# Optimization experiments

Measured on AMD Instinct MI355X. Metric: run time of the kernel, lower is better.

## Reference

```python
import jax, jax.numpy as jnp
import numpy as np

HIDDEN = 512
HEAD = 64
SEQ = 2048
CHUNK = 256
GAMMA = 0.96875
SCALE_BASE = 512.0


def _xpos(x, downscale):
    # x: [B, L, hd]; XPOS with offset=0 (scale rows == length, no trimming needed)
    B, L, hd = x.shape
    half = hd // 2
    scale_vec = (jnp.arange(0, hd, 2, dtype=jnp.float32) + 0.4 * hd) / (1.4 * hd)  # [half]
    power = jnp.arange(L, dtype=jnp.float32) / SCALE_BASE                          # [L]
    scale = scale_vec[None, :] ** power[:, None]                                   # [L, half]
    inv_freq = 1.0 / (10000.0 ** (jnp.arange(half, dtype=jnp.float32) / half))
    sinusoid = jnp.arange(L, dtype=jnp.float32)[:, None] * inv_freq[None, :]       # [L, half]
    sin, cos = jnp.sin(sinusoid), jnp.cos(sinusoid)
    if downscale:
        scale = 1.0 / scale
    # duplicate_interleave: repeat each column twice -> [L, hd]
    sin_f = jnp.repeat(sin * scale, 2, axis=-1)
    cos_f = jnp.repeat(cos * scale, 2, axis=-1)
    x1 = x[:, :, 0::2]
    x2 = x[:, :, 1::2]
    rot = jnp.stack((-x2, x1), axis=-1).reshape(B, L, hd)  # rotate_every_two
    return x * cos_f + rot * sin_f


def _D_parallel():
    # D[i, j] = gamma^|i-j| if j < (i//chunk + 1)*chunk else 0 (block-causal with in-chunk lookahead)
    i = jnp.arange(SEQ)[:, None]
    j = jnp.arange(SEQ)[None, :]
    j_max = (i // CHUNK + 1) * CHUNK
    decay = GAMMA ** jnp.abs(i - j).astype(jnp.float32)
    return jnp.where(j < j_max, decay, 0.0)  # gamma>0 so no NaNs to scrub


def setup_inputs() -> dict:
    key = jax.random.key(0)
    k1, k2, k3, k4 = jax.random.split(key, 4)
    X = jax.random.normal(k1, (8, SEQ, HIDDEN), dtype=jnp.float32)
    W_Q = jax.random.normal(k2, (HIDDEN, HEAD), dtype=jnp.float32) / HIDDEN
    W_K = jax.random.normal(k3, (HIDDEN, HEAD), dtype=jnp.float32) / HIDDEN
    W_V = jax.random.normal(k4, (HIDDEN, HEAD), dtype=jnp.float32) / HIDDEN
    return {"X": X, "W_Q": W_Q, "W_K": W_K, "W_V": W_V}


def reference(X, W_Q, W_K, W_V):
    Q = _xpos(X @ W_Q, downscale=False)   # [B, S, H]
    K = _xpos(X @ W_K, downscale=True)    # [B, S, H]
    V = X @ W_V                           # [B, S, V]
    D = _D_parallel()                     # [S, S]
    scores = jnp.einsum('bqh,bkh->bqk', Q, K) * D[None]
    return jnp.einsum('bqk,bkv->bqv', scores, V)
```

## Files before the change

kernel.cpp:

```cpp
#include <hip/hip_runtime.h>
#include <hip/hip_bf16.h>


typedef __attribute__((ext_vector_type(8))) short short8;
typedef __attribute__((ext_vector_type(4))) float floatx4;

#define LOG2GAMMA (-0.04580350f)

static __device__ __forceinline__ unsigned short f2bf(float f) {
    __hip_bfloat16 h = __float2bfloat16(f);
    return *reinterpret_cast<unsigned short*>(&h);
}


__global__ __launch_bounds__(256) void prep_kernel(
    const float* __restrict__ Wq, const float* __restrict__ Wk,
    const float* __restrict__ Wv,
    __hip_bfloat16* __restrict__ Wfrag, float* __restrict__ tabs)
{
    int idx = blockIdx.x * 256 + threadIdx.x;
    const int WF_N = 192 * 512;
    if (idx < WF_N) {
        int j    = idx & 7;
        int n15  = (idx >> 3) & 15;
        int quad = (idx >> 7) & 3;
        int kkg  = (idx >> 9) & 15;
        int tile = idx >> 13;
        int n = tile * 16 + n15;
        int k = kkg * 32 + quad * 8 + j;
        int m = n >> 6, c = n & 63;
        const float* W = (m == 0) ? Wq : ((m == 1) ? Wk : Wv);
        Wfrag[idx] = __float2bfloat16(W[k * 64 + c]);
    } else {
        int t2 = idx - WF_N;
        if (t2 < 4 * 2048 * 32) {
            int tab = t2 >> 16;
            int rem = t2 & 65535;
            int pos = rem >> 5;
            int t   = rem & 31;
            float inv_freq = powf(10000.0f, -(float)t / 32.0f);
            float sinus = (float)pos * inv_freq;
            float s = sinf(sinus), c = cosf(sinus);
            float sv = (2.0f * (float)t + 0.4f * 64.0f) / (1.4f * 64.0f);
            float power = (float)pos / 512.0f;
            float scl = powf(sv, (tab >= 2) ? -power : power);
            tabs[t2] = ((tab & 1) == 0) ? c * scl : s * scl;
        }
    }
}

__global__ __launch_bounds__(256, 4) void proj_kernel(
    const float* __restrict__ X, const __hip_bfloat16* __restrict__ Wfrag,
    const float* __restrict__ tabs,
    __hip_bfloat16* __restrict__ Qfrag, __hip_bfloat16* __restrict__ Kfrag,
    __hip_bfloat16* __restrict__ Vfrag)
{
    __shared__ __hip_bfloat16 smem[32 * 520];

    int tid = threadIdx.x;
    int r0 = blockIdx.x * 32;
    int w = tid >> 6, lane = tid & 63, quad = lane >> 4, l15 = lane & 15;
    int rh = w & 1, nh = w >> 1;

#pragma unroll
    for (int u = 0; u < 16; u++) {
        int f = u * 256 + tid;
        int row = f >> 7, c = f & 127;
        float4 v = *(const float4*)(X + (r0 + row) * 512 + c * 4);
        ushort4 pk;
        pk.x = f2bf(v.x); pk.y = f2bf(v.y); pk.z = f2bf(v.z); pk.w = f2bf(v.w);
        *(ushort4*)&smem[row * 520 + c * 4] = pk;
    }
    __syncthreads();

    floatx4 acc[6];
#pragma unroll
    for (int t = 0; t < 6; t++) acc[t] = (floatx4){0.f, 0.f, 0.f, 0.f};

#pragma unroll
    for (int ks = 0; ks < 16; ks++) {
        short8 a = *(const short8*)&smem[(rh * 16 + l15) * 520 + ks * 32 + quad * 8];
#pragma unroll
        for (int t = 0; t < 6; t++) {
            int tile = nh * 6 + t;
            short8 bfr = *(const short8*)(Wfrag + ((tile * 16 + ks) * 64 + lane) * 8);
            acc[t] = __builtin_amdgcn_mfma_f32_16x16x32_bf16(a, bfr, acc[t], 0, 0, 0);
        }
    }
    __syncthreads();

    __hip_bfloat16* bufQ = smem;
    __hip_bfloat16* bufK = smem + 2304;
    __hip_bfloat16* bufV = smem + 4608;
    int b = r0 >> 11, n0 = r0 & 2047;
    int rrow = rh * 16 + quad * 4;

#pragma unroll
    for (int tl = 0; tl < 6; tl++) {
        int t = nh * 6 + tl;
#pragma unroll
        for (int rg = 0; rg < 4; rg++) {
            int row = rrow + rg;
            int n = n0 + row;
            float val = acc[tl][rg];
            float prt = __shfl_xor(val, 1, 64);
            if (t < 4) {
                int ch = t * 16 + l15, tt = ch >> 1;
                float co = tabs[n * 32 + tt];
                float si = tabs[65536 + n * 32 + tt];
                float o = (l15 & 1) ? (val * co + prt * si) : (val * co - prt * si);
                bufQ[row * 72 + ch] = __float2bfloat16(o);
            } else if (t < 8) {
                int ch = (t - 4) * 16 + l15, tt = ch >> 1;
                float co = tabs[131072 + n * 32 + tt];
                float si = tabs[196608 + n * 32 + tt];
                float o = (l15 & 1) ? (val * co + prt * si) : (val * co - prt * si);
                bufK[row * 72 + ch] = __float2bfloat16(o);
            } else {
                int ch = (t - 8) * 16 + l15;
                bufV[ch * 40 + row] = __float2bfloat16(val);
            }
        }
    }
    __syncthreads();

    {
        int tile2 = tid >> 7, kk = (tid >> 6) & 1, ln = tid & 63;
        int q2 = ln >> 4, m15 = ln & 15;
        size_t qkbase = ((((size_t)b * 128 + (n0 >> 4) + tile2) * 2 + kk) * 64 + ln) * 8;
        uint4 vq = *(const uint4*)&bufQ[(tile2 * 16 + m15) * 72 + kk * 32 + q2 * 8];
        *(uint4*)(Qfrag + qkbase) = vq;
        uint4 vk = *(const uint4*)&bufK[(tile2 * 16 + m15) * 72 + kk * 32 + q2 * 8];
        *(uint4*)(Kfrag + qkbase) = vk;
        int t2 = tid >> 6;
        uint4 vv = *(const uint4*)&bufV[(t2 * 16 + m15) * 40 + q2 * 8];
        *(uint4*)(Vfrag + ((((size_t)b * 64 + (n0 >> 5)) * 4 + t2) * 64 + ln) * 8) = vv;
    }
}

__global__ __launch_bounds__(256, 3) void attn_kernel(
    const __hip_bfloat16* __restrict__ Qfrag, const __hip_bfloat16* __restrict__ Kfrag,
    const __hip_bfloat16* __restrict__ Vfrag, float* __restrict__ out)
{
    __shared__ __hip_bfloat16 lp[4][16 * 264];

    int tid = threadIdx.x;
    int b = blockIdx.x >> 6, qt = blockIdx.x & 63;
    int q0 = qt * 32, qc = q0 >> 8;
    int w = tid >> 6, lane = tid & 63, quad = lane >> 4, l15 = lane & 15;
    int qh = w >> 1, h = w & 1;
    int qt16 = (q0 >> 4) + qh;

    short8 qf[2];
#pragma unroll
    for (int kk = 0; kk < 2; kk++)
        qf[kk] = *(const short8*)(Qfrag + ((((size_t)b * 128 + qt16) * 2 + kk) * 64 + lane) * 8);

    __hip_bfloat16* P = &lp[w][0];

    floatx4 o[4];
#pragma unroll
    for (int t = 0; t < 4; t++) o[t] = (floatx4){0.f, 0.f, 0.f, 0.f};

    int kc0 = (qc >= 3) ? (qc - 3) : 0;
    for (int kc = kc0 + h; kc <= qc; kc += 2) {
        floatx4 s[16];
#pragma unroll
        for (int t = 0; t < 16; t++) s[t] = (floatx4){0.f, 0.f, 0.f, 0.f};
#pragma unroll
        for (int t = 0; t < 16; t++) {
#pragma unroll
            for (int kk = 0; kk < 2; kk++) {
                short8 bfr = *(const short8*)(Kfrag +
                    ((((size_t)b * 128 + kc * 16 + t) * 2 + kk) * 64 + lane) * 8);
                s[t] = __builtin_amdgcn_mfma_f32_16x16x32_bf16(qf[kk], bfr, s[t], 0, 0, 0);
            }
        }

        int i0 = q0 + qh * 16 + quad * 4;
        int kbase = kc * 256;
#pragma unroll
        for (int t = 0; t < 16; t++) {
            int j = kbase + t * 16 + l15;
#pragma unroll
            for (int rg = 0; rg < 4; rg++) {
                int d = i0 + rg - j; d = (d < 0) ? -d : d;
                float p = s[t][rg] * exp2f(LOG2GAMMA * (float)d);
                P[(quad * 4 + rg) * 264 + t * 16 + l15] = __float2bfloat16(p);
            }
        }

#pragma unroll
        for (int ks = 0; ks < 8; ks++) {
            short8 a = *(const short8*)&P[l15 * 264 + ks * 32 + quad * 8];
#pragma unroll
            for (int t2 = 0; t2 < 4; t2++) {
                short8 bfr = *(const short8*)(Vfrag +
                    ((((size_t)b * 64 + kc * 8 + ks) * 4 + t2) * 64 + lane) * 8);
                o[t2] = __builtin_amdgcn_mfma_f32_16x16x32_bf16(a, bfr, o[t2], 0, 0, 0);
            }
        }
    }

    float* mine = (float*)&lp[w][0];
    float* part = (float*)&lp[w ^ 1][0];
    if (h == 1) {
#pragma unroll
        for (int t2 = 0; t2 < 4; t2++)
#pragma unroll
            for (int rg = 0; rg < 4; rg++)
                mine[(quad * 4 + rg) * 64 + t2 * 16 + l15] = o[t2][rg];
    }
    __syncthreads();
    if (h == 0) {
        int rbase = b * 2048 + q0 + qh * 16 + quad * 4;
#pragma unroll
        for (int t2 = 0; t2 < 4; t2++)
#pragma unroll
            for (int rg = 0; rg < 4; rg++)
                out[(size_t)(rbase + rg) * 64 + t2 * 16 + l15] =
                    o[t2][rg] + part[(quad * 4 + rg) * 64 + t2 * 16 + l15];
    }
}

extern "C" void kernel_launch(void* const* d_in, const int* in_sizes, int n_in,
                              void* d_out, int out_size, void* d_ws, size_t ws_size,
                              hipStream_t stream) {
    const float* X  = (const float*)d_in[0];
    const float* Wq = (const float*)d_in[1];
    const float* Wk = (const float*)d_in[2];
    const float* Wv = (const float*)d_in[3];
    float* out = (float*)d_out;

    char* ws = (char*)d_ws;
    __hip_bfloat16* Wfrag = (__hip_bfloat16*)(ws);
    float*          tabs  = (float*)(ws + 196608);
    __hip_bfloat16* Qfrag = (__hip_bfloat16*)(ws + 1245184);
    __hip_bfloat16* Kfrag = (__hip_bfloat16*)(ws + 3342336);
    __hip_bfloat16* Vfrag = (__hip_bfloat16*)(ws + 5439488);

    prep_kernel<<<1408, 256, 0, stream>>>(Wq, Wk, Wv, Wfrag, tabs);
    proj_kernel<<<512, 256, 0, stream>>>(X, Wfrag, tabs, Qfrag, Kfrag, Vfrag);
    attn_kernel<<<512, 256, 0, stream>>>(Qfrag, Kfrag, Vfrag, out);
}
```

Baseline: 128.2 us.

## Replace off-diagonal chunk attention with chunkwise recurrent KV state

Attention is reformulated in the retention style. Each chunk's decayed K^T V state is precomputed by a new zk kernel. The attention kernel then handles only the diagonal chunk explicitly and adds contributions from up to three previous chunks through a decay-scaled Q times a combined state, summed with gamma^256 weights. This removes most of the off-diagonal QK and PV MFMA work, at the cost of an extra launch, extra workspace, and bf16 rounding of the decayed K and the combined state, which adds precision risk.

New measurement: 111.8 us. -12.8%, faster.

```diff
diff --git a/kernel.cpp b/kernel.cpp
--- a/kernel.cpp
+++ b/kernel.cpp
@@ -6,6 +6,7 @@
 typedef __attribute__((ext_vector_type(4))) float floatx4;
 
 #define LOG2GAMMA (-0.04580350f)
+#define GINV      (1.0f / 0.96875f)
 
 static __device__ __forceinline__ unsigned short f2bf(float f) {
     __hip_bfloat16 h = __float2bfloat16(f);
@@ -53,7 +54,8 @@
     const float* __restrict__ X, const __hip_bfloat16* __restrict__ Wfrag,
     const float* __restrict__ tabs,
     __hip_bfloat16* __restrict__ Qfrag, __hip_bfloat16* __restrict__ Kfrag,
-    __hip_bfloat16* __restrict__ Vfrag)
+    __hip_bfloat16* __restrict__ Vfrag, __hip_bfloat16* __restrict__ Qsfrag,
+    __hip_bfloat16* __restrict__ Ktfrag)
 {
     __shared__ __hip_bfloat16 smem[32 * 520];
 
@@ -89,9 +91,10 @@
     }
     __syncthreads();
 
-    __hip_bfloat16* bufQ = smem;
-    __hip_bfloat16* bufK = smem + 2304;
-    __hip_bfloat16* bufV = smem + 4608;
+    __hip_bfloat16* bufQ  = smem;
+    __hip_bfloat16* bufK  = smem + 2304;
+    __hip_bfloat16* bufV  = smem + 4608;
+    __hip_bfloat16* bufQs = smem + 7168;
     int b = r0 >> 11, n0 = r0 & 2047;
     int rrow = rh * 16 + quad * 4;
 
@@ -110,6 +113,8 @@
                 float si = tabs[65536 + n * 32 + tt];
                 float o = (l15 & 1) ? (val * co + prt * si) : (val * co - prt * si);
                 bufQ[row * 72 + ch] = __float2bfloat16(o);
+                float qs = exp2f(LOG2GAMMA * (float)((n & 255) + 1));
+                bufQs[row * 72 + ch] = __float2bfloat16(o * qs);
             } else if (t < 8) {
                 int ch = (t - 4) * 16 + l15, tt = ch >> 1;
                 float co = tabs[131072 + n * 32 + tt];
@@ -130,96 +135,186 @@
         size_t qkbase = ((((size_t)b * 128 + (n0 >> 4) + tile2) * 2 + kk) * 64 + ln) * 8;
         uint4 vq = *(const uint4*)&bufQ[(tile2 * 16 + m15) * 72 + kk * 32 + q2 * 8];
         *(uint4*)(Qfrag + qkbase) = vq;
+        uint4 vqs = *(const uint4*)&bufQs[(tile2 * 16 + m15) * 72 + kk * 32 + q2 * 8];
+        *(uint4*)(Qsfrag + qkbase) = vqs;
         uint4 vk = *(const uint4*)&bufK[(tile2 * 16 + m15) * 72 + kk * 32 + q2 * 8];
         *(uint4*)(Kfrag + qkbase) = vk;
         int t2 = tid >> 6;
         uint4 vv = *(const uint4*)&bufV[(t2 * 16 + m15) * 40 + q2 * 8];
         *(uint4*)(Vfrag + ((((size_t)b * 64 + (n0 >> 5)) * 4 + t2) * 64 + ln) * 8) = vv;
     }
-}
-
-__global__ __launch_bounds__(256, 3) void attn_kernel(
+    {
+        int wdt = tid >> 6, ln2 = tid & 63;
+        int q2 = ln2 >> 4, m15 = ln2 & 15;
+        int jb0 = (n0 & 255) + q2 * 8;
+        float sc = exp2f(LOG2GAMMA * (float)(255 - jb0));
+        short8 pk;
+#pragma unroll
+        for (int jj = 0; jj < 8; jj++) {
+            float v = __bfloat162float(bufK[(q2 * 8 + jj) * 72 + wdt * 16 + m15]) * sc;
+            pk[jj] = (short)f2bf(v);
+            sc *= GINV;
+        }
+        int c = n0 >> 8, ksg = (n0 >> 5) & 7;
+        *(short8*)(Ktfrag + ((((size_t)(b * 8 + c) * 4 + wdt) * 8 + ksg) * 64 + ln2) * 8) = pk;
+    }
+}
+
+__global__ __launch_bounds__(256, 2) void zk_kernel(
+    const __hip_bfloat16* __restrict__ Ktfrag,
+    const __hip_bfloat16* __restrict__ Vfrag, float* __restrict__ Zf)
+{
+    __shared__ float zz[64 * 68];
+
+    int tid = threadIdx.x;
+    int b = blockIdx.x >> 3, c = blockIdx.x & 7;
+    int w = tid >> 6, lane = tid & 63, quad = lane >> 4, l15 = lane & 15;
+
+    floatx4 acc[4];
+#pragma unroll
+    for (int t = 0; t < 4; t++) acc[t] = (floatx4){0.f, 0.f, 0.f, 0.f};
+
+#pragma unroll
+    for (int ks = 0; ks < 8; ks++) {
+        short8 a = *(const short8*)(Ktfrag +
+            ((((size_t)(b * 8 + c) * 4 + w) * 8 + ks) * 64 + lane) * 8);
+#pragma unroll
+        for (int vt = 0; vt < 4; vt++) {
+            short8 bfr = *(const short8*)(Vfrag +
+                ((((size_t)b * 64 + c * 8 + ks) * 4 + vt) * 64 + lane) * 8);
+            acc[vt] = __builtin_amdgcn_mfma_f32_16x16x32_bf16(a, bfr, acc[vt], 0, 0, 0);
+        }
+    }
+#pragma unroll
+    for (int vt = 0; vt < 4; vt++)
+#pragma unroll
+        for (int rg = 0; rg < 4; rg++)
+            zz[(w * 16 + quad * 4 + rg) * 68 + vt * 16 + l15] = acc[vt][rg];
+    __syncthreads();
+
+    {
+        int vt = tid >> 6;
+#pragma unroll
+        for (int kk = 0; kk < 2; kk++) {
+            float v[8];
+#pragma unroll
+            for (int jd = 0; jd < 8; jd++)
+                v[jd] = zz[(kk * 32 + quad * 8 + jd) * 68 + vt * 16 + l15];
+            float* zp = Zf + (((((size_t)(b * 8 + c) * 4 + vt) * 2 + kk) * 64 + lane) * 8);
+            *(float4*)zp       = (float4){v[0], v[1], v[2], v[3]};
+            *(float4*)(zp + 4) = (float4){v[4], v[5], v[6], v[7]};
+        }
+    }
+}
+
+__global__ __launch_bounds__(128, 4) void attn_kernel(
     const __hip_bfloat16* __restrict__ Qfrag, const __hip_bfloat16* __restrict__ Kfrag,
-    const __hip_bfloat16* __restrict__ Vfrag, float* __restrict__ out)
+    const __hip_bfloat16* __restrict__ Vfrag, const __hip_bfloat16* __restrict__ Qsfrag,
+    const float* __restrict__ Zf, float* __restrict__ out)
 {
-    __shared__ __hip_bfloat16 lp[4][16 * 264];
+    __shared__ __hip_bfloat16 P[2 * 16 * 132];
+    __shared__ float obuf[16 * 68];
 
     int tid = threadIdx.x;
-    int b = blockIdx.x >> 6, qt = blockIdx.x & 63;
-    int q0 = qt * 32, qc = q0 >> 8;
-    int w = tid >> 6, lane = tid & 63, quad = lane >> 4, l15 = lane & 15;
-    int qh = w >> 1, h = w & 1;
-    int qt16 = (q0 >> 4) + qh;
+    int b = blockIdx.x >> 7, qt = blockIdx.x & 127;
+    int qc = qt >> 4;
+    int h = tid >> 6, lane = tid & 63, quad = lane >> 4, l15 = lane & 15;
+    __hip_bfloat16* Pw = P + h * 2112;
 
     short8 qf[2];
 #pragma unroll
     for (int kk = 0; kk < 2; kk++)
-        qf[kk] = *(const short8*)(Qfrag + ((((size_t)b * 128 + qt16) * 2 + kk) * 64 + lane) * 8);
-
-    __hip_bfloat16* P = &lp[w][0];
+        qf[kk] = *(const short8*)(Qfrag + (((size_t)(b * 128 + qt) * 2 + kk) * 64 + lane) * 8);
 
     floatx4 o[4];
 #pragma unroll
     for (int t = 0; t < 4; t++) o[t] = (floatx4){0.f, 0.f, 0.f, 0.f};
 
-    int kc0 = (qc >= 3) ? (qc - 3) : 0;
-    for (int kc = kc0 + h; kc <= qc; kc += 2) {
-        floatx4 s[16];
-#pragma unroll
-        for (int t = 0; t < 16; t++) s[t] = (floatx4){0.f, 0.f, 0.f, 0.f};
-#pragma unroll
-        for (int t = 0; t < 16; t++) {
+    int il0 = (qt & 15) * 16 + quad * 4;
+
+#pragma unroll
+    for (int g = 0; g < 2; g++) {
+        floatx4 s[4];
+#pragma unroll
+        for (int t = 0; t < 4; t++) s[t] = (floatx4){0.f, 0.f, 0.f, 0.f};
+#pragma unroll
+        for (int t = 0; t < 4; t++) {
+            int kt = qc * 16 + h * 8 + g * 4 + t;
 #pragma unroll
             for (int kk = 0; kk < 2; kk++) {
                 short8 bfr = *(const short8*)(Kfrag +
-                    ((((size_t)b * 128 + kc * 16 + t) * 2 + kk) * 64 + lane) * 8);
+                    (((size_t)(b * 128 + kt) * 2 + kk) * 64 + lane) * 8);
                 s[t] = __builtin_amdgcn_mfma_f32_16x16x32_bf16(qf[kk], bfr, s[t], 0, 0, 0);
             }
         }
-
-        int i0 = q0 + qh * 16 + quad * 4;
-        int kbase = kc * 256;
-#pragma unroll
-        for (int t = 0; t < 16; t++) {
-            int j = kbase + t * 16 + l15;
+#pragma unroll
+        for (int t = 0; t < 4; t++) {
+            int jl = h * 128 + (g * 4 + t) * 16 + l15;
 #pragma unroll
             for (int rg = 0; rg < 4; rg++) {
-                int d = i0 + rg - j; d = (d < 0) ? -d : d;
+                int d = il0 + rg - jl; d = (d < 0) ? -d : d;
                 float p = s[t][rg] * exp2f(LOG2GAMMA * (float)d);
-                P[(quad * 4 + rg) * 264 + t * 16 + l15] = __float2bfloat16(p);
+                Pw[(quad * 4 + rg) * 132 + (g * 4 + t) * 16 + l15] = __float2bfloat16(p);
             }
         }
-
-#pragma unroll
-        for (int ks = 0; ks < 8; ks++) {
-            short8 a = *(const short8*)&P[l15 * 264 + ks * 32 + quad * 8];
-#pragma unroll
-            for (int t2 = 0; t2 < 4; t2++) {
-                short8 bfr = *(const short8*)(Vfrag +
-                    ((((size_t)b * 64 + kc * 8 + ks) * 4 + t2) * 64 + lane) * 8);
-                o[t2] = __builtin_amdgcn_mfma_f32_16x16x32_bf16(a, bfr, o[t2], 0, 0, 0);
+    }
+#pragma unroll
+    for (int ks = 0; ks < 4; ks++) {
+        short8 a = *(const short8*)&Pw[l15 * 132 + ks * 32 + quad * 8];
+#pragma unroll
+        for (int vt = 0; vt < 4; vt++) {
+            short8 bfr = *(const short8*)(Vfrag +
+                ((((size_t)b * 64 + qc * 8 + h * 4 + ks) * 4 + vt) * 64 + lane) * 8);
+            o[vt] = __builtin_amdgcn_mfma_f32_16x16x32_bf16(a, bfr, o[vt], 0, 0, 0);
+        }
+    }
+
+    if (qc > 0) {
+        short8 aq = *(const short8*)(Qsfrag +
+            (((size_t)(b * 128 + qt) * 2 + h) * 64 + lane) * 8);
+        int nz = (qc < 3) ? qc : 3;
+        float cm0 = 1.0f;
+        float cm1 = exp2f(LOG2GAMMA * 256.0f);
+        float cm2 = exp2f(LOG2GAMMA * 512.0f);
+#pragma unroll
+        for (int vt = 0; vt < 4; vt++) {
+            float hv[8];
+#pragma unroll
+            for (int jd = 0; jd < 8; jd++) hv[jd] = 0.f;
+            for (int m = 0; m < nz; m++) {
+                float cm = (m == 0) ? cm0 : ((m == 1) ? cm1 : cm2);
+                const float* zp = Zf +
+                    (((((size_t)(b * 8 + qc - 1 - m) * 4 + vt) * 2 + h) * 64 + lane) * 8);
+                float4 z0 = *(const float4*)zp;
+                float4 z1 = *(const float4*)(zp + 4);
+                hv[0] += cm * z0.x; hv[1] += cm * z0.y;
+                hv[2] += cm * z0.z; hv[3] += cm * z0.w;
+                hv[4] += cm * z1.x; hv[5] += cm * z1.y;
+                hv[6] += cm * z1.z; hv[7] += cm * z1.w;
             }
-        }
-    }
-
-    float* mine = (float*)&lp[w][0];
-    float* part = (float*)&lp[w ^ 1][0];
+            short8 hb;
+#pragma unroll
+            for (int jd = 0; jd < 8; jd++) hb[jd] = (short)f2bf(hv[jd]);
+            o[vt] = __builtin_amdgcn_mfma_f32_16x16x32_bf16(aq, hb, o[vt], 0, 0, 0);
+        }
+    }
+
     if (h == 1) {
 #pragma unroll
-        for (int t2 = 0; t2 < 4; t2++)
+        for (int vt = 0; vt < 4; vt++)
 #pragma unroll
             for (int rg = 0; rg < 4; rg++)
-                mine[(quad * 4 + rg) * 64 + t2 * 16 + l15] = o[t2][rg];
+                obuf[(quad * 4 + rg) * 68 + vt * 16 + l15] = o[vt][rg];
     }
     __syncthreads();
     if (h == 0) {
-        int rbase = b * 2048 + q0 + qh * 16 + quad * 4;
-#pragma unroll
-        for (int t2 = 0; t2 < 4; t2++)
+        int rbase = b * 2048 + qt * 16 + quad * 4;
+#pragma unroll
+        for (int vt = 0; vt < 4; vt++)
 #pragma unroll
             for (int rg = 0; rg < 4; rg++)
-                out[(size_t)(rbase + rg) * 64 + t2 * 16 + l15] =
-                    o[t2][rg] + part[(quad * 4 + rg) * 64 + t2 * 16 + l15];
+                out[(size_t)(rbase + rg) * 64 + vt * 16 + l15] =
+                    o[vt][rg] + obuf[(quad * 4 + rg) * 68 + vt * 16 + l15];
     }
 }
 
@@ -233,13 +328,18 @@
     float* out = (float*)d_out;
 
     char* ws = (char*)d_ws;
-    __hip_bfloat16* Wfrag = (__hip_bfloat16*)(ws);
-    float*          tabs  = (float*)(ws + 196608);
-    __hip_bfloat16* Qfrag = (__hip_bfloat16*)(ws + 1245184);
-    __hip_bfloat16* Kfrag = (__hip_bfloat16*)(ws + 3342336);
-    __hip_bfloat16* Vfrag = (__hip_bfloat16*)(ws + 5439488);
+    __hip_bfloat16* Wfrag  = (__hip_bfloat16*)(ws);
+    float*          tabs   = (float*)(ws + 196608);
+    __hip_bfloat16* Qfrag  = (__hip_bfloat16*)(ws + 1245184);
+    __hip_bfloat16* Kfrag  = (__hip_bfloat16*)(ws + 3342336);
+    __hip_bfloat16* Vfrag  = (__hip_bfloat16*)(ws + 5439488);
+    __hip_bfloat16* Qsfrag = (__hip_bfloat16*)(ws + 7536640);
+    __hip_bfloat16* Ktfrag = (__hip_bfloat16*)(ws + 9633792);
+    float*          Zf     = (float*)(ws + 11730944);
 
     prep_kernel<<<1408, 256, 0, stream>>>(Wq, Wk, Wv, Wfrag, tabs);
-    proj_kernel<<<512, 256, 0, stream>>>(X, Wfrag, tabs, Qfrag, Kfrag, Vfrag);
-    attn_kernel<<<512, 256, 0, stream>>>(Qfrag, Kfrag, Vfrag, out);
-}
+    proj_kernel<<<512, 256, 0, stream>>>(X, Wfrag, tabs, Qfrag, Kfrag, Vfrag,
+                                         Qsfrag, Ktfrag);
+    zk_kernel<<<64, 256, 0, stream>>>(Ktfrag, Vfrag, Zf);
+    attn_kernel<<<1024, 128, 0, stream>>>(Qfrag, Kfrag, Vfrag, Qsfrag, Zf, out);
+}
```
